# Optimization experiments

Hardware: AMD Instinct MI355X
Metric: run time of the kernel (lower is better)

The kernel has to match this reference:

```python
import jax, jax.numpy as jnp
import numpy as np

IN_CH = 1024
INTER_CH = 512
NUM_EXPERTS = 128
B, S = 16, 4096  # T = B*S = 65536 tokens, 512 tokens/expert


def setup_inputs() -> dict:
    key = jax.random.key(0)
    kx, kp, k1w, k1b, k2w, k2b, k3w, k3b = jax.random.split(key, 8)
    T = B * S
    x = jax.random.normal(kx, (B, S, IN_CH), dtype=jnp.float32)
    # Mirror torch: indices = randperm(T) % E; idxs = indices.argsort() (stable)
    perm = jax.random.permutation(kp, T)
    expert_assign = perm % NUM_EXPERTS
    idxs = jnp.argsort(expert_assign, stable=True).astype(jnp.int64)
    # BatchLinear params initialized with randn, matching the torch module
    w1_w = jax.random.normal(k1w, (NUM_EXPERTS, INTER_CH, IN_CH), dtype=jnp.float32)
    w1_b = jax.random.normal(k1b, (NUM_EXPERTS, INTER_CH), dtype=jnp.float32)
    w2_w = jax.random.normal(k2w, (NUM_EXPERTS, IN_CH, INTER_CH), dtype=jnp.float32)
    w2_b = jax.random.normal(k2b, (NUM_EXPERTS, IN_CH), dtype=jnp.float32)
    w3_w = jax.random.normal(k3w, (NUM_EXPERTS, INTER_CH, IN_CH), dtype=jnp.float32)
    w3_b = jax.random.normal(k3b, (NUM_EXPERTS, INTER_CH), dtype=jnp.float32)
    return {"x": x, "idxs": idxs, "w1_w": w1_w, "w1_b": w1_b,
            "w2_w": w2_w, "w2_b": w2_b, "w3_w": w3_w, "w3_b": w3_b}


def reference(x, idxs, w1_w, w1_b, w2_w, w2_b, w3_w, w3_b):
    Bx, Sx, C = x.shape
    E = w1_w.shape[0]
    xf = x.reshape(Bx * Sx, C)            # [T, C]
    # dispatch: gather tokens grouped by expert -> [E, T/E, C]
    xs = xf[idxs].reshape(E, -1, C)
    # SwiGLU FFN, batched over experts
    h1 = jnp.einsum('etc,efc->etf', xs, w1_w) + w1_b[:, None, :]  # [E, T/E, F]
    h3 = jnp.einsum('etc,efc->etf', xs, w3_w) + w3_b[:, None, :]
    h = jax.nn.silu(h1) * h3
    out = jnp.einsum('etf,ecf->etc', h, w2_w) + w2_b[:, None, :]  # [E, T/E, C]
    # combine: scatter tokens back to original order
    out = out.reshape(Bx * Sx, C)
    inv = jnp.argsort(idxs)
    return out[inv].reshape(Bx, Sx, C)
```

## Files before the change

kernel.cpp:

```cpp
#include <hip/hip_runtime.h>

#define IN_CH 1024
#define INTER 512
#define NEXP  128
#define TPE   512

typedef __bf16 bf16x8  __attribute__((ext_vector_type(8)));
typedef __bf16 bf16x4v __attribute__((ext_vector_type(4)));
typedef float  f32x4   __attribute__((ext_vector_type(4)));

#define GLOAD(dst, p) \
  asm volatile("global_load_dwordx4 %0, %1, off" : "=&v"(dst) : "v"(p))

#define VM_WAIT() do { \
  asm volatile("s_waitcnt vmcnt(0)" ::: "memory"); \
  __builtin_amdgcn_sched_barrier(0); } while (0)

#define PHASE_SYNC() do { \
  __builtin_amdgcn_s_barrier(); \
  asm volatile("s_waitcnt lgkmcnt(0)" ::: "memory"); \
  __builtin_amdgcn_sched_barrier(0); \
  __builtin_amdgcn_s_setprio(1); } while (0)
#define PHASE_END() do { \
  __builtin_amdgcn_s_setprio(0); \
  __builtin_amdgcn_s_barrier(); } while (0)

__global__ __launch_bounds__(512) void moe_h_kernel(
    const float* __restrict__ x, const int* __restrict__ idxs,
    const float* __restrict__ w1w, const float* __restrict__ w1b,
    const float* __restrict__ w3w, const float* __restrict__ w3b,
    __bf16* __restrict__ hbuf)
{
  __shared__ __align__(16) ushort sA [2][128*64];
  __shared__ __align__(16) ushort sB1[2][128*64];
  __shared__ __align__(16) ushort sB3[2][128*64];

  const int blk = (blockIdx.x & 7) * (NEXP*16/8) + (blockIdx.x >> 3);
  const int e   = blk >> 4;
  const int tl  = blk & 15;
  const int tm  = tl >> 2, tn = tl & 3;

  const int tid  = threadIdx.x;
  const int lane = tid & 63;
  const int wid  = tid >> 6;
  const int wm   = wid >> 1;
  const int wn   = wid & 1;

  const int r0 = tid >> 4;
  const int c4 = tid & 15;

  const float* aptr[4];
#pragma unroll
  for (int i = 0; i < 4; ++i) {
    const int tok = idxs[e*TPE + tm*128 + r0 + 32*i];
    aptr[i] = x + (size_t)tok*IN_CH + (c4<<2);
  }
  const float* b1p = w1w + ((size_t)e*INTER + tn*128 + r0)*IN_CH + (c4<<2);
  const float* b3p = w3w + ((size_t)e*INTER + tn*128 + r0)*IN_CH + (c4<<2);

  const int swz = ((((c4>>1) ^ (r0&7))<<3) | ((c4&1)<<2));

  f32x4 acc1[2][4], acc3[2][4];
#pragma unroll
  for (int a = 0; a < 2; ++a)
#pragma unroll
    for (int b = 0; b < 4; ++b) {
      acc1[a][b] = (f32x4){0.f,0.f,0.f,0.f};
      acc3[a][b] = (f32x4){0.f,0.f,0.f,0.f};
    }

  f32x4 xv[4], v1[4], v3[4];

  auto loads = [&](int kof) {
#pragma unroll
    for (int i = 0; i < 4; ++i) {
      GLOAD(xv[i], aptr[i] + kof);
      GLOAD(v1[i], b1p + (size_t)(32*i)*IN_CH + kof);
      GLOAD(v3[i], b3p + (size_t)(32*i)*IN_CH + kof);
    }
  };
  auto cvt4 = [](const f32x4& v) {
    bf16x4v b;
    b[0]=(__bf16)v[0]; b[1]=(__bf16)v[1]; b[2]=(__bf16)v[2]; b[3]=(__bf16)v[3];
    return b;
  };
  auto stores = [&](int buf) {
    VM_WAIT();
#pragma unroll
    for (int i = 0; i < 4; ++i) {
      const int ro = (r0 + 32*i)*64 + swz;
      *(bf16x4v*)&sA [buf][ro] = cvt4(xv[i]);
      *(bf16x4v*)&sB1[buf][ro] = cvt4(v1[i]);
      *(bf16x4v*)&sB3[buf][ro] = cvt4(v3[i]);
    }
  };
  auto mfma_tile = [&](int buf) {
#pragma unroll
    for (int ks = 0; ks < 2; ++ks) {
      bf16x8 af[2], bq[4], bt[4];
      const int k8 = (ks<<2) + (lane>>4);
#pragma unroll
      for (int mi = 0; mi < 2; ++mi) {
        const int r = wm*32 + mi*16 + (lane&15);
        af[mi] = *(const bf16x8*)&sA[buf][r*64 + ((k8 ^ (r&7))<<3)];
      }
#pragma unroll
      for (int ni = 0; ni < 4; ++ni) {
        const int r   = wn*64 + ni*16 + (lane&15);
        const int off = r*64 + ((k8 ^ (r&7))<<3);
        bq[ni] = *(const bf16x8*)&sB1[buf][off];
        bt[ni] = *(const bf16x8*)&sB3[buf][off];
      }
#pragma unroll
      for (int mi = 0; mi < 2; ++mi)
#pragma unroll
        for (int ni = 0; ni < 4; ++ni) {
          acc1[mi][ni] = __builtin_amdgcn_mfma_f32_16x16x32_bf16(af[mi], bq[ni], acc1[mi][ni], 0, 0, 0);
          acc3[mi][ni] = __builtin_amdgcn_mfma_f32_16x16x32_bf16(af[mi], bt[ni], acc3[mi][ni], 0, 0, 0);
        }
    }
  };

  loads(0);
  stores(0);
  loads(64);
  asm volatile("s_waitcnt lgkmcnt(0)" ::: "memory");
  __builtin_amdgcn_s_barrier();

  int cur = 0;
  const int NT = IN_CH/64;
  for (int kt = 0; kt < NT; ++kt) {
    if (kt < NT - 1) stores(cur ^ 1);
    if (kt < NT - 2) loads((kt+2)*64);
    __builtin_amdgcn_s_setprio(1);
    mfma_tile(cur);
    __builtin_amdgcn_s_setprio(0);
    asm volatile("s_waitcnt lgkmcnt(0)" ::: "memory");
    __builtin_amdgcn_s_barrier();
    cur ^= 1;
  }

  const int rowbase = tm*128 + wm*32;
  const int colbase = tn*128 + wn*64;
#pragma unroll
  for (int ni = 0; ni < 4; ++ni) {
    const int fc = colbase + ni*16 + (lane&15);
    const float b1v = w1b[e*INTER + fc];
    const float b3v = w3b[e*INTER + fc];
#pragma unroll
    for (int mi = 0; mi < 2; ++mi) {
#pragma unroll
      for (int j = 0; j < 4; ++j) {
        const int rl = rowbase + mi*16 + ((lane>>4)<<2) + j;
        const float h1 = acc1[mi][ni][j] + b1v;
        const float h3 = acc3[mi][ni][j] + b3v;
        const float s  = h1 / (1.0f + __expf(-h1));
        hbuf[((size_t)e*TPE + rl)*INTER + fc] = (__bf16)(s * h3);
      }
    }
  }
}

__global__ __launch_bounds__(512) void moe_out_kernel(
    const __bf16* __restrict__ hbuf, const float* __restrict__ w2w,
    const float* __restrict__ w2b, const int* __restrict__ idxs,
    float* __restrict__ out)
{
  __shared__ __align__(16) ushort sA[2][128*64];
  __shared__ __align__(16) ushort sB[2][128*64];

  const int blk = (blockIdx.x & 7) * (NEXP*32/8) + (blockIdx.x >> 3);
  const int e   = blk >> 5;
  const int tl  = blk & 31;
  const int tm  = tl >> 3, tn = tl & 7;

  const int tid  = threadIdx.x;
  const int lane = tid & 63;
  const int wid  = tid >> 6;
  const int wm   = wid >> 1;
  const int wn   = wid & 1;

  const int rA   = tid >> 3;
  const int c8   = tid & 7;
  const int swzA = ((c8 ^ (rA&7))<<3);
  const __bf16* ap = hbuf + ((size_t)e*TPE + tm*128 + rA)*INTER + (c8<<3);

  const int r0   = tid >> 4;
  const int c4   = tid & 15;
  const int swzB = ((((c4>>1) ^ (r0&7))<<3) | ((c4&1)<<2));
  const float* bp = w2w + ((size_t)e*IN_CH + tn*128 + r0)*INTER + (c4<<2);

  f32x4 acc[2][4];
#pragma unroll
  for (int a = 0; a < 2; ++a)
#pragma unroll
    for (int b = 0; b < 4; ++b) acc[a][b] = (f32x4){0.f,0.f,0.f,0.f};

  uint4  hv[2];
  float4 wv[4];

  auto loads = [&](int kof) {
#pragma unroll
    for (int i = 0; i < 2; ++i)
      hv[i] = *(const uint4*)(ap + (size_t)(64*i)*INTER + kof);
#pragma unroll
    for (int i = 0; i < 4; ++i)
      wv[i] = *(const float4*)(bp + (size_t)(32*i)*INTER + kof);
  };
  auto stores = [&](int buf) {
#pragma unroll
    for (int i = 0; i < 2; ++i)
      *(uint4*)&sA[buf][(rA + 64*i)*64 + swzA] = hv[i];
#pragma unroll
    for (int i = 0; i < 4; ++i) {
      bf16x4v b;
      b[0]=(__bf16)wv[i].x; b[1]=(__bf16)wv[i].y; b[2]=(__bf16)wv[i].z; b[3]=(__bf16)wv[i].w;
      *(bf16x4v*)&sB[buf][(r0 + 32*i)*64 + swzB] = b;
    }
  };
  auto rdA = [&](int buf, int ks, bf16x8 af[2]) {
    const int k8 = (ks<<2) + (lane>>4);
#pragma unroll
    for (int mi = 0; mi < 2; ++mi) {
      const int r = wm*32 + mi*16 + (lane&15);
      af[mi] = *(const bf16x8*)&sA[buf][r*64 + ((k8 ^ (r&7))<<3)];
    }
  };
  auto rdB = [&](int buf, int ks, bf16x8 bfr[4]) {
    const int k8 = (ks<<2) + (lane>>4);
#pragma unroll
    for (int ni = 0; ni < 4; ++ni) {
      const int r = wn*64 + ni*16 + (lane&15);
      bfr[ni] = *(const bf16x8*)&sB[buf][r*64 + ((k8 ^ (r&7))<<3)];
    }
  };

  loads(0);
  stores(0);
  loads(64);
  asm volatile("s_waitcnt lgkmcnt(0)" ::: "memory");
  __builtin_amdgcn_s_barrier();

  int cur = 0;
  const int NT = INTER/64;
  for (int kt = 0; kt < NT; ++kt) {
    bf16x8 af[2], bfr[4];

    rdA(cur, 0, af);
    rdB(cur, 0, bfr);
    if (kt < NT - 1) stores(cur ^ 1);
    PHASE_SYNC();
#pragma unroll
    for (int mi = 0; mi < 2; ++mi)
#pragma unroll
      for (int ni = 0; ni < 4; ++ni)
        acc[mi][ni] = __builtin_amdgcn_mfma_f32_16x16x32_bf16(af[mi], bfr[ni], acc[mi][ni], 0, 0, 0);
    PHASE_END();

    rdA(cur, 1, af);
    rdB(cur, 1, bfr);
    if (kt < NT - 2) loads((kt+2)*64);
    PHASE_SYNC();
#pragma unroll
    for (int mi = 0; mi < 2; ++mi)
#pragma unroll
      for (int ni = 0; ni < 4; ++ni)
        acc[mi][ni] = __builtin_amdgcn_mfma_f32_16x16x32_bf16(af[mi], bfr[ni], acc[mi][ni], 0, 0, 0);
    PHASE_END();

    cur ^= 1;
  }

  const int rowbase = tm*128 + wm*32;
  const int colbase = tn*128 + wn*64;
  float b2v[4];
#pragma unroll
  for (int ni = 0; ni < 4; ++ni)
    b2v[ni] = w2b[e*IN_CH + colbase + ni*16 + (lane&15)];
#pragma unroll
  for (int mi = 0; mi < 2; ++mi) {
#pragma unroll
    for (int j = 0; j < 4; ++j) {
      const int rl  = rowbase + mi*16 + ((lane>>4)<<2) + j;
      const int tok = idxs[e*TPE + rl];
      float* orow = out + (size_t)tok*IN_CH;
#pragma unroll
      for (int ni = 0; ni < 4; ++ni)
        orow[colbase + ni*16 + (lane&15)] = acc[mi][ni][j] + b2v[ni];
    }
  }
}

extern "C" void kernel_launch(void* const* d_in, const int* in_sizes, int n_in,
                              void* d_out, int out_size, void* d_ws, size_t ws_size,
                              hipStream_t stream) {
  const float* x    = (const float*)d_in[0];
  const int*   idxs = (const int*)d_in[1];
  const float* w1w  = (const float*)d_in[2];
  const float* w1b  = (const float*)d_in[3];
  const float* w2w  = (const float*)d_in[4];
  const float* w2b  = (const float*)d_in[5];
  const float* w3w  = (const float*)d_in[6];
  const float* w3b  = (const float*)d_in[7];
  float*  out  = (float*)d_out;
  __bf16* hbuf = (__bf16*)d_ws;

  moe_h_kernel<<<dim3(NEXP*16), dim3(512), 0, stream>>>(x, idxs, w1w, w1b, w3w, w3b, hbuf);
  moe_out_kernel<<<dim3(NEXP*32), dim3(512), 0, stream>>>(hbuf, w2w, w2b, idxs, out);
}
```

Baseline: 490.2 us.

## Split first GEMM main loop into four barrier-synchronized phases interleaving loads and MFMAs

```diff
diff --git a/kernel.cpp b/kernel.cpp
--- a/kernel.cpp
+++ b/kernel.cpp
@@ -71,74 +71,111 @@
 
   f32x4 xv[4], v1[4], v3[4];
 
-  auto loads = [&](int kof) {
-#pragma unroll
-    for (int i = 0; i < 4; ++i) {
-      GLOAD(xv[i], aptr[i] + kof);
-      GLOAD(v1[i], b1p + (size_t)(32*i)*IN_CH + kof);
-      GLOAD(v3[i], b3p + (size_t)(32*i)*IN_CH + kof);
-    }
+  auto loadsH1 = [&](int kof) {
+    GLOAD(xv[0], aptr[0] + kof);
+    GLOAD(xv[1], aptr[1] + kof);
+    GLOAD(xv[2], aptr[2] + kof);
+    GLOAD(xv[3], aptr[3] + kof);
+    GLOAD(v1[0], b1p + kof);
+    GLOAD(v1[1], b1p + (size_t)32*IN_CH + kof);
+  };
+  auto loadsH2 = [&](int kof) {
+    GLOAD(v1[2], b1p + (size_t)64*IN_CH + kof);
+    GLOAD(v1[3], b1p + (size_t)96*IN_CH + kof);
+    GLOAD(v3[0], b3p + kof);
+    GLOAD(v3[1], b3p + (size_t)32*IN_CH + kof);
+    GLOAD(v3[2], b3p + (size_t)64*IN_CH + kof);
+    GLOAD(v3[3], b3p + (size_t)96*IN_CH + kof);
   };
   auto cvt4 = [](const f32x4& v) {
     bf16x4v b;
     b[0]=(__bf16)v[0]; b[1]=(__bf16)v[1]; b[2]=(__bf16)v[2]; b[3]=(__bf16)v[3];
     return b;
   };
-  auto stores = [&](int buf) {
-    VM_WAIT();
-#pragma unroll
-    for (int i = 0; i < 4; ++i) {
-      const int ro = (r0 + 32*i)*64 + swz;
-      *(bf16x4v*)&sA [buf][ro] = cvt4(xv[i]);
-      *(bf16x4v*)&sB1[buf][ro] = cvt4(v1[i]);
-      *(bf16x4v*)&sB3[buf][ro] = cvt4(v3[i]);
-    }
-  };
-  auto mfma_tile = [&](int buf) {
-#pragma unroll
-    for (int ks = 0; ks < 2; ++ks) {
-      bf16x8 af[2], bq[4], bt[4];
-      const int k8 = (ks<<2) + (lane>>4);
-#pragma unroll
-      for (int mi = 0; mi < 2; ++mi) {
-        const int r = wm*32 + mi*16 + (lane&15);
-        af[mi] = *(const bf16x8*)&sA[buf][r*64 + ((k8 ^ (r&7))<<3)];
-      }
-#pragma unroll
-      for (int ni = 0; ni < 4; ++ni) {
-        const int r   = wn*64 + ni*16 + (lane&15);
-        const int off = r*64 + ((k8 ^ (r&7))<<3);
-        bq[ni] = *(const bf16x8*)&sB1[buf][off];
-        bt[ni] = *(const bf16x8*)&sB3[buf][off];
-      }
-#pragma unroll
-      for (int mi = 0; mi < 2; ++mi)
-#pragma unroll
-        for (int ni = 0; ni < 4; ++ni) {
-          acc1[mi][ni] = __builtin_amdgcn_mfma_f32_16x16x32_bf16(af[mi], bq[ni], acc1[mi][ni], 0, 0, 0);
-          acc3[mi][ni] = __builtin_amdgcn_mfma_f32_16x16x32_bf16(af[mi], bt[ni], acc3[mi][ni], 0, 0, 0);
-        }
-    }
-  };
-
-  loads(0);
-  stores(0);
-  loads(64);
+  auto storeA = [&](int buf) {
+#pragma unroll
+    for (int i = 0; i < 4; ++i)
+      *(bf16x4v*)&sA[buf][(r0 + 32*i)*64 + swz] = cvt4(xv[i]);
+  };
+  auto storeB1 = [&](int buf) {
+#pragma unroll
+    for (int i = 0; i < 4; ++i)
+      *(bf16x4v*)&sB1[buf][(r0 + 32*i)*64 + swz] = cvt4(v1[i]);
+  };
+  auto storeB3 = [&](int buf) {
+#pragma unroll
+    for (int i = 0; i < 4; ++i)
+      *(bf16x4v*)&sB3[buf][(r0 + 32*i)*64 + swz] = cvt4(v3[i]);
+  };
+  auto rdA = [&](int buf, int ks, bf16x8 af[2]) {
+    const int k8 = (ks<<2) + (lane>>4);
+#pragma unroll
+    for (int mi = 0; mi < 2; ++mi) {
+      const int r = wm*32 + mi*16 + (lane&15);
+      af[mi] = *(const bf16x8*)&sA[buf][r*64 + ((k8 ^ (r&7))<<3)];
+    }
+  };
+  auto rdBh = [&](int buf, int ks, int nh, bf16x8 bq[2], bf16x8 bt[2]) {
+    const int k8 = (ks<<2) + (lane>>4);
+#pragma unroll
+    for (int nl = 0; nl < 2; ++nl) {
+      const int r   = wn*64 + (nh*2 + nl)*16 + (lane&15);
+      const int off = r*64 + ((k8 ^ (r&7))<<3);
+      bq[nl] = *(const bf16x8*)&sB1[buf][off];
+      bt[nl] = *(const bf16x8*)&sB3[buf][off];
+    }
+  };
+
+#define MFMA8(NH) \
+  _Pragma("unroll") \
+  for (int mi = 0; mi < 2; ++mi) \
+    _Pragma("unroll") \
+    for (int nl = 0; nl < 2; ++nl) { \
+      acc1[mi][(NH)*2+nl] = __builtin_amdgcn_mfma_f32_16x16x32_bf16(af[mi], bq[nl], acc1[mi][(NH)*2+nl], 0, 0, 0); \
+      acc3[mi][(NH)*2+nl] = __builtin_amdgcn_mfma_f32_16x16x32_bf16(af[mi], bt[nl], acc3[mi][(NH)*2+nl], 0, 0, 0); \
+    }
+
+  loadsH1(0); loadsH2(0);
+  VM_WAIT();
+  storeA(0); storeB1(0); storeB3(0);
+  loadsH1(64); loadsH2(64);
   asm volatile("s_waitcnt lgkmcnt(0)" ::: "memory");
   __builtin_amdgcn_s_barrier();
 
   int cur = 0;
   const int NT = IN_CH/64;
   for (int kt = 0; kt < NT; ++kt) {
-    if (kt < NT - 1) stores(cur ^ 1);
-    if (kt < NT - 2) loads((kt+2)*64);
-    __builtin_amdgcn_s_setprio(1);
-    mfma_tile(cur);
-    __builtin_amdgcn_s_setprio(0);
-    asm volatile("s_waitcnt lgkmcnt(0)" ::: "memory");
-    __builtin_amdgcn_s_barrier();
+    bf16x8 af[2], bq[2], bt[2];
+
+    rdA(cur, 0, af);
+    rdBh(cur, 0, 0, bq, bt);
+    if (kt < NT - 1) { VM_WAIT(); storeA(cur ^ 1); storeB1(cur ^ 1); }
+    PHASE_SYNC();
+    MFMA8(0)
+    PHASE_END();
+
+    rdBh(cur, 0, 1, bq, bt);
+    if (kt < NT - 1) storeB3(cur ^ 1);
+    if (kt < NT - 2) loadsH1((kt+2)*64);
+    PHASE_SYNC();
+    MFMA8(1)
+    PHASE_END();
+
+    rdA(cur, 1, af);
+    rdBh(cur, 1, 0, bq, bt);
+    if (kt < NT - 2) loadsH2((kt+2)*64);
+    PHASE_SYNC();
+    MFMA8(0)
+    PHASE_END();
+
+    rdBh(cur, 1, 1, bq, bt);
+    PHASE_SYNC();
+    MFMA8(1)
+    PHASE_END();
+
     cur ^= 1;
   }
+#undef MFMA8
 
   const int rowbase = tm*128 + wm*32;
   const int colbase = tn*128 + wn*64;
```

Result: slower. 569.0 us (+16.1%).

## Load W1/W3 fragments directly into registers, share only token tile in LDS

Applied to the files above, without the earlier changes.

```diff
diff --git a/kernel.cpp b/kernel.cpp
--- a/kernel.cpp
+++ b/kernel.cpp
@@ -31,9 +31,7 @@
     const float* __restrict__ w3w, const float* __restrict__ w3b,
     __bf16* __restrict__ hbuf)
 {
-  __shared__ __align__(16) ushort sA [2][128*64];
-  __shared__ __align__(16) ushort sB1[2][128*64];
-  __shared__ __align__(16) ushort sB3[2][128*64];
+  __shared__ __align__(16) ushort sA[2][128*64];
 
   const int blk = (blockIdx.x & 7) * (NEXP*16/8) + (blockIdx.x >> 3);
   const int e   = blk >> 4;
@@ -42,12 +40,11 @@
 
   const int tid  = threadIdx.x;
   const int lane = tid & 63;
-  const int wid  = tid >> 6;
-  const int wm   = wid >> 1;
-  const int wn   = wid & 1;
+  const int w    = tid >> 6;
 
   const int r0 = tid >> 4;
   const int c4 = tid & 15;
+  const int swz = ((((c4>>1) ^ (r0&7))<<3) | ((c4&1)<<2));
 
   const float* aptr[4];
 #pragma unroll
@@ -55,108 +52,109 @@
     const int tok = idxs[e*TPE + tm*128 + r0 + 32*i];
     aptr[i] = x + (size_t)tok*IN_CH + (c4<<2);
   }
-  const float* b1p = w1w + ((size_t)e*INTER + tn*128 + r0)*IN_CH + (c4<<2);
-  const float* b3p = w3w + ((size_t)e*INTER + tn*128 + r0)*IN_CH + (c4<<2);
-
-  const int swz = ((((c4>>1) ^ (r0&7))<<3) | ((c4&1)<<2));
-
-  f32x4 acc1[2][4], acc3[2][4];
-#pragma unroll
-  for (int a = 0; a < 2; ++a)
-#pragma unroll
-    for (int b = 0; b < 4; ++b) {
-      acc1[a][b] = (f32x4){0.f,0.f,0.f,0.f};
-      acc3[a][b] = (f32x4){0.f,0.f,0.f,0.f};
-    }
-
-  f32x4 xv[4], v1[4], v3[4];
-
-  auto loads = [&](int kof) {
-#pragma unroll
-    for (int i = 0; i < 4; ++i) {
-      GLOAD(xv[i], aptr[i] + kof);
-      GLOAD(v1[i], b1p + (size_t)(32*i)*IN_CH + kof);
-      GLOAD(v3[i], b3p + (size_t)(32*i)*IN_CH + kof);
-    }
+
+  const size_t frow = (size_t)e*INTER + tn*128 + w*16 + (lane&15);
+  const float* b1p = w1w + frow*IN_CH + ((lane>>4)<<3);
+  const float* b3p = w3w + frow*IN_CH + ((lane>>4)<<3);
+
+  f32x4 acc1[8], acc3[8];
+#pragma unroll
+  for (int a = 0; a < 8; ++a) {
+    acc1[a] = (f32x4){0.f,0.f,0.f,0.f};
+    acc3[a] = (f32x4){0.f,0.f,0.f,0.f};
+  }
+
+  f32x4 xv[4];
+  f32x4 q1[2][2], q3[2][2], r1[2][2], r3[2][2];
+
+  auto loadsA = [&](int kof) {
+#pragma unroll
+    for (int i = 0; i < 4; ++i) GLOAD(xv[i], aptr[i] + kof);
   };
   auto cvt4 = [](const f32x4& v) {
     bf16x4v b;
     b[0]=(__bf16)v[0]; b[1]=(__bf16)v[1]; b[2]=(__bf16)v[2]; b[3]=(__bf16)v[3];
     return b;
   };
-  auto stores = [&](int buf) {
+  auto storeA = [&](int buf) {
+#pragma unroll
+    for (int i = 0; i < 4; ++i)
+      *(bf16x4v*)&sA[buf][(r0 + 32*i)*64 + swz] = cvt4(xv[i]);
+  };
+  auto loadsB = [&](f32x4 bq[2][2], f32x4 bt[2][2], int kof) {
+#pragma unroll
+    for (int ks = 0; ks < 2; ++ks) {
+      GLOAD(bq[ks][0], b1p + kof + ks*32);
+      GLOAD(bq[ks][1], b1p + kof + ks*32 + 4);
+      GLOAD(bt[ks][0], b3p + kof + ks*32);
+      GLOAD(bt[ks][1], b3p + kof + ks*32 + 4);
+    }
+  };
+  auto cvt8 = [](const f32x4& lo, const f32x4& hi) {
+    bf16x8 r;
+    r[0]=(__bf16)lo[0]; r[1]=(__bf16)lo[1]; r[2]=(__bf16)lo[2]; r[3]=(__bf16)lo[3];
+    r[4]=(__bf16)hi[0]; r[5]=(__bf16)hi[1]; r[6]=(__bf16)hi[2]; r[7]=(__bf16)hi[3];
+    return r;
+  };
+
+  const int NT = IN_CH/64;
+
+  auto kstep = [&](int kt, f32x4 cq[2][2], f32x4 ct[2][2],
+                   f32x4 nq[2][2], f32x4 nt[2][2]) {
+    const int cur = kt & 1;
     VM_WAIT();
-#pragma unroll
-    for (int i = 0; i < 4; ++i) {
-      const int ro = (r0 + 32*i)*64 + swz;
-      *(bf16x4v*)&sA [buf][ro] = cvt4(xv[i]);
-      *(bf16x4v*)&sB1[buf][ro] = cvt4(v1[i]);
-      *(bf16x4v*)&sB3[buf][ro] = cvt4(v3[i]);
-    }
-  };
-  auto mfma_tile = [&](int buf) {
+    if (kt < NT - 1) storeA(cur ^ 1);
+    if (kt < NT - 2) loadsA((kt+2)*64);
+    if (kt < NT - 1) loadsB(nq, nt, (kt+1)*64);
+    bf16x8 f1[2], f3[2];
 #pragma unroll
     for (int ks = 0; ks < 2; ++ks) {
-      bf16x8 af[2], bq[4], bt[4];
+      f1[ks] = cvt8(cq[ks][0], cq[ks][1]);
+      f3[ks] = cvt8(ct[ks][0], ct[ks][1]);
+    }
+    __builtin_amdgcn_s_setprio(1);
+#pragma unroll
+    for (int ks = 0; ks < 2; ++ks) {
       const int k8 = (ks<<2) + (lane>>4);
 #pragma unroll
-      for (int mi = 0; mi < 2; ++mi) {
-        const int r = wm*32 + mi*16 + (lane&15);
-        af[mi] = *(const bf16x8*)&sA[buf][r*64 + ((k8 ^ (r&7))<<3)];
+      for (int mi = 0; mi < 8; ++mi) {
+        const int r = mi*16 + (lane&15);
+        const bf16x8 af = *(const bf16x8*)&sA[cur][r*64 + ((k8 ^ (r&7))<<3)];
+        acc1[mi] = __builtin_amdgcn_mfma_f32_16x16x32_bf16(af, f1[ks], acc1[mi], 0, 0, 0);
+        acc3[mi] = __builtin_amdgcn_mfma_f32_16x16x32_bf16(af, f3[ks], acc3[mi], 0, 0, 0);
       }
-#pragma unroll
-      for (int ni = 0; ni < 4; ++ni) {
-        const int r   = wn*64 + ni*16 + (lane&15);
-        const int off = r*64 + ((k8 ^ (r&7))<<3);
-        bq[ni] = *(const bf16x8*)&sB1[buf][off];
-        bt[ni] = *(const bf16x8*)&sB3[buf][off];
-      }
-#pragma unroll
-      for (int mi = 0; mi < 2; ++mi)
-#pragma unroll
-        for (int ni = 0; ni < 4; ++ni) {
-          acc1[mi][ni] = __builtin_amdgcn_mfma_f32_16x16x32_bf16(af[mi], bq[ni], acc1[mi][ni], 0, 0, 0);
-          acc3[mi][ni] = __builtin_amdgcn_mfma_f32_16x16x32_bf16(af[mi], bt[ni], acc3[mi][ni], 0, 0, 0);
-        }
-    }
-  };
-
-  loads(0);
-  stores(0);
-  loads(64);
-  asm volatile("s_waitcnt lgkmcnt(0)" ::: "memory");
-  __builtin_amdgcn_s_barrier();
-
-  int cur = 0;
-  const int NT = IN_CH/64;
-  for (int kt = 0; kt < NT; ++kt) {
-    if (kt < NT - 1) stores(cur ^ 1);
-    if (kt < NT - 2) loads((kt+2)*64);
-    __builtin_amdgcn_s_setprio(1);
-    mfma_tile(cur);
+    }
     __builtin_amdgcn_s_setprio(0);
     asm volatile("s_waitcnt lgkmcnt(0)" ::: "memory");
     __builtin_amdgcn_s_barrier();
-    cur ^= 1;
-  }
-
-  const int rowbase = tm*128 + wm*32;
-  const int colbase = tn*128 + wn*64;
-#pragma unroll
-  for (int ni = 0; ni < 4; ++ni) {
-    const int fc = colbase + ni*16 + (lane&15);
-    const float b1v = w1b[e*INTER + fc];
-    const float b3v = w3b[e*INTER + fc];
-#pragma unroll
-    for (int mi = 0; mi < 2; ++mi) {
-#pragma unroll
-      for (int j = 0; j < 4; ++j) {
-        const int rl = rowbase + mi*16 + ((lane>>4)<<2) + j;
-        const float h1 = acc1[mi][ni][j] + b1v;
-        const float h3 = acc3[mi][ni][j] + b3v;
-        const float s  = h1 / (1.0f + __expf(-h1));
-        hbuf[((size_t)e*TPE + rl)*INTER + fc] = (__bf16)(s * h3);
-      }
+  };
+
+  loadsB(q1, q3, 0);
+  loadsA(0);
+  VM_WAIT();
+  storeA(0);
+  loadsA(64);
+  asm volatile("s_waitcnt lgkmcnt(0)" ::: "memory");
+  __builtin_amdgcn_s_barrier();
+
+  for (int k2 = 0; k2 < NT/2; ++k2) {
+    kstep(2*k2,     q1, q3, r1, r3);
+    kstep(2*k2 + 1, r1, r3, q1, q3);
+  }
+
+  const int fc = tn*128 + w*16 + (lane&15);
+  const float b1v = w1b[e*INTER + fc];
+  const float b3v = w3b[e*INTER + fc];
+  const int rowbase = tm*128;
+#pragma unroll
+  for (int mi = 0; mi < 8; ++mi) {
+#pragma unroll
+    for (int j = 0; j < 4; ++j) {
+      const int rl = rowbase + mi*16 + ((lane>>4)<<2) + j;
+      const float h1 = acc1[mi][j] + b1v;
+      const float h3 = acc3[mi][j] + b3v;
+      const float s  = h1 / (1.0f + __expf(-h1));
+      hbuf[((size_t)e*TPE + rl)*INTER + fc] = (__bf16)(s * h3);
     }
   }
 }
```

Result: slower. 528.1 us (+7.7%).

## Load hbuf directly into LDS and widen h-kernel staging to 8-element rows

Applied to the files above, without the earlier changes.

```diff
diff --git a/kernel.cpp b/kernel.cpp
--- a/kernel.cpp
+++ b/kernel.cpp
@@ -24,6 +24,11 @@
 #define PHASE_END() do { \
   __builtin_amdgcn_s_setprio(0); \
   __builtin_amdgcn_s_barrier(); } while (0)
+
+#define GLDS16(gsrc, ldst) \
+  __builtin_amdgcn_global_load_lds( \
+      (const __attribute__((address_space(1))) unsigned int*)(gsrc), \
+      (__attribute__((address_space(3))) unsigned int*)(ldst), 16, 0, 0)
 
 __global__ __launch_bounds__(512) void moe_h_kernel(
     const float* __restrict__ x, const int* __restrict__ idxs,
@@ -46,19 +51,20 @@
   const int wm   = wid >> 1;
   const int wn   = wid & 1;
 
-  const int r0 = tid >> 4;
-  const int c4 = tid & 15;
-
-  const float* aptr[4];
-#pragma unroll
-  for (int i = 0; i < 4; ++i) {
-    const int tok = idxs[e*TPE + tm*128 + r0 + 32*i];
-    aptr[i] = x + (size_t)tok*IN_CH + (c4<<2);
-  }
-  const float* b1p = w1w + ((size_t)e*INTER + tn*128 + r0)*IN_CH + (c4<<2);
-  const float* b3p = w3w + ((size_t)e*INTER + tn*128 + r0)*IN_CH + (c4<<2);
-
-  const int swz = ((((c4>>1) ^ (r0&7))<<3) | ((c4&1)<<2));
+  const int rA = tid >> 3;
+  const int c  = tid & 7;
+  const int swzc = ((c ^ (rA&7))<<3);
+  const int so0 = rA*64 + swzc;
+  const int so1 = (rA+64)*64 + swzc;
+
+  const int tok0 = idxs[e*TPE + tm*128 + rA];
+  const int tok1 = idxs[e*TPE + tm*128 + rA + 64];
+  const float* ap0 = x + (size_t)tok0*IN_CH + (c<<3);
+  const float* ap1 = x + (size_t)tok1*IN_CH + (c<<3);
+  const float* q0p = w1w + ((size_t)e*INTER + tn*128 + rA)*IN_CH + (c<<3);
+  const float* q1p = q0p + (size_t)64*IN_CH;
+  const float* t0p = w3w + ((size_t)e*INTER + tn*128 + rA)*IN_CH + (c<<3);
+  const float* t1p = t0p + (size_t)64*IN_CH;
 
   f32x4 acc1[2][4], acc3[2][4];
 #pragma unroll
@@ -69,30 +75,30 @@
       acc3[a][b] = (f32x4){0.f,0.f,0.f,0.f};
     }
 
-  f32x4 xv[4], v1[4], v3[4];
+  f32x4 a0l,a0h, a1l,a1h, q0l,q0h, q1l,q1h, t0l,t0h, t1l,t1h;
 
   auto loads = [&](int kof) {
-#pragma unroll
-    for (int i = 0; i < 4; ++i) {
-      GLOAD(xv[i], aptr[i] + kof);
-      GLOAD(v1[i], b1p + (size_t)(32*i)*IN_CH + kof);
-      GLOAD(v3[i], b3p + (size_t)(32*i)*IN_CH + kof);
-    }
-  };
-  auto cvt4 = [](const f32x4& v) {
-    bf16x4v b;
-    b[0]=(__bf16)v[0]; b[1]=(__bf16)v[1]; b[2]=(__bf16)v[2]; b[3]=(__bf16)v[3];
-    return b;
+    GLOAD(a0l, ap0 + kof); GLOAD(a0h, ap0 + kof + 4);
+    GLOAD(a1l, ap1 + kof); GLOAD(a1h, ap1 + kof + 4);
+    GLOAD(q0l, q0p + kof); GLOAD(q0h, q0p + kof + 4);
+    GLOAD(q1l, q1p + kof); GLOAD(q1h, q1p + kof + 4);
+    GLOAD(t0l, t0p + kof); GLOAD(t0h, t0p + kof + 4);
+    GLOAD(t1l, t1p + kof); GLOAD(t1h, t1p + kof + 4);
+  };
+  auto cvt8 = [](const f32x4& lo, const f32x4& hi) {
+    bf16x8 r;
+    r[0]=(__bf16)lo[0]; r[1]=(__bf16)lo[1]; r[2]=(__bf16)lo[2]; r[3]=(__bf16)lo[3];
+    r[4]=(__bf16)hi[0]; r[5]=(__bf16)hi[1]; r[6]=(__bf16)hi[2]; r[7]=(__bf16)hi[3];
+    return r;
   };
   auto stores = [&](int buf) {
     VM_WAIT();
-#pragma unroll
-    for (int i = 0; i < 4; ++i) {
-      const int ro = (r0 + 32*i)*64 + swz;
-      *(bf16x4v*)&sA [buf][ro] = cvt4(xv[i]);
-      *(bf16x4v*)&sB1[buf][ro] = cvt4(v1[i]);
-      *(bf16x4v*)&sB3[buf][ro] = cvt4(v3[i]);
-    }
+    *(bf16x8*)&sA [buf][so0] = cvt8(a0l, a0h);
+    *(bf16x8*)&sA [buf][so1] = cvt8(a1l, a1h);
+    *(bf16x8*)&sB1[buf][so0] = cvt8(q0l, q0h);
+    *(bf16x8*)&sB1[buf][so1] = cvt8(q1l, q1h);
+    *(bf16x8*)&sB3[buf][so0] = cvt8(t0l, t0h);
+    *(bf16x8*)&sB3[buf][so1] = cvt8(t1l, t1h);
   };
   auto mfma_tile = [&](int buf) {
 #pragma unroll
@@ -180,10 +186,13 @@
   const int wm   = wid >> 1;
   const int wn   = wid & 1;
 
-  const int rA   = tid >> 3;
-  const int c8   = tid & 7;
-  const int swzA = ((c8 ^ (rA&7))<<3);
-  const __bf16* ap = hbuf + ((size_t)e*TPE + tm*128 + rA)*INTER + (c8<<3);
+  const int arow0 = wid*16 + (lane>>3);
+  const int asc0  = (lane&7) ^ (arow0&7);
+  const int asc1  = (lane&7) ^ ((arow0+8)&7);
+  const __bf16* ag0 = hbuf + ((size_t)e*TPE + tm*128 + arow0    )*INTER + (asc0<<3);
+  const __bf16* ag1 = hbuf + ((size_t)e*TPE + tm*128 + arow0 + 8)*INTER + (asc1<<3);
+  const int aslot0 = (wid*128)      * 8;
+  const int aslot1 = (wid*128 + 64) * 8;
 
   const int r0   = tid >> 4;
   const int c4   = tid & 15;
@@ -196,21 +205,18 @@
 #pragma unroll
     for (int b = 0; b < 4; ++b) acc[a][b] = (f32x4){0.f,0.f,0.f,0.f};
 
-  uint4  hv[2];
   float4 wv[4];
 
-  auto loads = [&](int kof) {
-#pragma unroll
-    for (int i = 0; i < 2; ++i)
-      hv[i] = *(const uint4*)(ap + (size_t)(64*i)*INTER + kof);
+  auto gldsA = [&](int buf, int kof) {
+    GLDS16(ag0 + kof, &sA[buf][aslot0]);
+    GLDS16(ag1 + kof, &sA[buf][aslot1]);
+  };
+  auto loadsB = [&](int kof) {
 #pragma unroll
     for (int i = 0; i < 4; ++i)
       wv[i] = *(const float4*)(bp + (size_t)(32*i)*INTER + kof);
   };
-  auto stores = [&](int buf) {
-#pragma unroll
-    for (int i = 0; i < 2; ++i)
-      *(uint4*)&sA[buf][(rA + 64*i)*64 + swzA] = hv[i];
+  auto storesB = [&](int buf) {
 #pragma unroll
     for (int i = 0; i < 4; ++i) {
       bf16x4v b;
@@ -235,9 +241,11 @@
     }
   };
 
-  loads(0);
-  stores(0);
-  loads(64);
+  gldsA(0, 0);
+  loadsB(0);
+  VM_WAIT();
+  storesB(0);
+  loadsB(64);
   asm volatile("s_waitcnt lgkmcnt(0)" ::: "memory");
   __builtin_amdgcn_s_barrier();
 
@@ -248,7 +256,13 @@
 
     rdA(cur, 0, af);
     rdB(cur, 0, bfr);
-    if (kt < NT - 1) stores(cur ^ 1);
+    if (kt < NT - 1) {
+      VM_WAIT();
+      storesB(cur ^ 1);
+      gldsA(cur ^ 1, (kt+1)*64);
+      __builtin_amdgcn_sched_barrier(0);
+    }
+    if (kt < NT - 2) loadsB((kt+2)*64);
     PHASE_SYNC();
 #pragma unroll
     for (int mi = 0; mi < 2; ++mi)
@@ -259,14 +273,16 @@
 
     rdA(cur, 1, af);
     rdB(cur, 1, bfr);
-    if (kt < NT - 2) loads((kt+2)*64);
     PHASE_SYNC();
 #pragma unroll
     for (int mi = 0; mi < 2; ++mi)
 #pragma unroll
       for (int ni = 0; ni < 4; ++ni)
         acc[mi][ni] = __builtin_amdgcn_mfma_f32_16x16x32_bf16(af[mi], bfr[ni], acc[mi][ni], 0, 0, 0);
-    PHASE_END();
+    __builtin_amdgcn_s_setprio(0);
+    if (kt < NT - 2)      asm volatile("s_waitcnt vmcnt(4)" ::: "memory");
+    else if (kt < NT - 1) asm volatile("s_waitcnt vmcnt(0)" ::: "memory");
+    __builtin_amdgcn_s_barrier();
 
     cur ^= 1;
   }
```

After: 483.5 us, median of 5. No clear change (-1.4%).
